# Optimization experiments

Measured on AMD Instinct MI355X. Metric: run time of the kernel, lower is better.

The kernel has to match this reference:

```python
import jax, jax.numpy as jnp
import numpy as np

B, P, ENC = 64, 49, 1280
T, V, E, H, A = 25, 10000, 512, 1024, 512


def setup_inputs() -> dict:
    key = jax.random.key(0)
    ks = jax.random.split(key, 20)
    s = 0.02
    return {
        "encoder_out": jax.random.normal(ks[0], (B, P, ENC), jnp.float32),
        "captions": jax.random.randint(ks[1], (B, T), 0, V, jnp.int32),
        "embed": jax.random.normal(ks[2], (V, E), jnp.float32) * s,
        "W_eatt": jax.random.normal(ks[3], (A, ENC), jnp.float32) * s,
        "b_eatt": jnp.zeros((A,), jnp.float32),
        "W_datt": jax.random.normal(ks[4], (A, H), jnp.float32) * s,
        "b_datt": jnp.zeros((A,), jnp.float32),
        "W_fatt": jax.random.normal(ks[5], (1, A), jnp.float32) * s,
        "b_fatt": jnp.zeros((1,), jnp.float32),
        "W_ih": jax.random.normal(ks[6], (4 * H, E + ENC), jnp.float32) * s,
        "b_ih": jnp.zeros((4 * H,), jnp.float32),
        "W_hh": jax.random.normal(ks[7], (4 * H, H), jnp.float32) * s,
        "b_hh": jnp.zeros((4 * H,), jnp.float32),
        "W_h0": jax.random.normal(ks[8], (H, ENC), jnp.float32) * s,
        "b_h0": jnp.zeros((H,), jnp.float32),
        "W_c0": jax.random.normal(ks[9], (H, ENC), jnp.float32) * s,
        "b_c0": jnp.zeros((H,), jnp.float32),
        "W_out": jax.random.normal(ks[10], (V, H), jnp.float32) * s,
        "b_out": jnp.zeros((V,), jnp.float32),
    }


def reference(encoder_out, captions, embed, W_eatt, b_eatt, W_datt, b_datt,
              W_fatt, b_fatt, W_ih, b_ih, W_hh, b_hh, W_h0, b_h0, W_c0, b_c0,
              W_out, b_out):
    emb = embed[captions]                       # [B,T,E]
    mean_enc = encoder_out.mean(axis=1)         # [B,ENC]
    h0 = mean_enc @ W_h0.T + b_h0               # [B,H]
    c0 = mean_enc @ W_c0.T + b_c0
    # encoder-side attention projection is step-invariant; hoist out of loop
    att1 = encoder_out @ W_eatt.T + b_eatt      # [B,P,A]
    nH = h0.shape[-1]

    def step(carry, x_t):
        h, c = carry
        att2 = h @ W_datt.T + b_datt                          # [B,A]
        e = (jax.nn.relu(att1 + att2[:, None, :]) @ W_fatt.T + b_fatt)[..., 0]  # [B,P]
        alpha = jax.nn.softmax(e, axis=1)
        ctx = jnp.einsum('bp,bpe->be', alpha, encoder_out)    # [B,ENC]
        gin = jnp.concatenate([x_t, ctx], axis=1)             # [B,E+ENC]
        gates = gin @ W_ih.T + b_ih + h @ W_hh.T + b_hh       # [B,4H]
        i, f, g, o = jnp.split(gates, 4, axis=1)
        c_new = jax.nn.sigmoid(f) * c + jax.nn.sigmoid(i) * jnp.tanh(g)
        h_new = jax.nn.sigmoid(o) * jnp.tanh(c_new)
        preds = h_new @ W_out.T + b_out                       # dropout in eval mode = identity
        return (h_new, c_new), preds

    xs = jnp.swapaxes(emb[:, :-1, :], 0, 1)     # [T-1,B,E]
    _, preds = jax.lax.scan(step, (h0, c0), xs)
    return jnp.swapaxes(preds, 0, 1)            # [B,T-1,V]
```

## Files before the change

### kernel.cpp

```cpp
#include <hip/hip_runtime.h>
#include <hip/hip_bf16.h>

typedef float  v4f __attribute__((ext_vector_type(4)));
typedef short  v8s __attribute__((ext_vector_type(8)));
typedef int    v4i __attribute__((ext_vector_type(4)));

#define DEV static __device__ __forceinline__

DEV float bf2f(unsigned short u) {
    union { unsigned int i; float f; } x; x.i = ((unsigned int)u) << 16; return x.f;
}
DEV unsigned short f2bf(float f) {
    union { float f; unsigned int i; } x; x.f = f;
    unsigned int r = x.i + 0x7fff + ((x.i >> 16) & 1);
    return (unsigned short)(r >> 16);
}
DEV float sigm(float x) { return 1.f / (1.f + __expf(-x)); }

__global__ __launch_bounds__(256) void uber_init(
    const float* __restrict__ Wih, const float* __restrict__ Whh,
    const float* __restrict__ bih, const float* __restrict__ bhh,
    const float* __restrict__ WoutF, const float* __restrict__ WeattF,
    const float* __restrict__ WdattF, const float* __restrict__ Wh0F,
    const float* __restrict__ Wc0F, const float* __restrict__ enc,
    const int* __restrict__ caps, const float* __restrict__ embed,
    unsigned short* __restrict__ Wz, unsigned short* __restrict__ Woutb,
    unsigned short* __restrict__ Weattb, unsigned short* __restrict__ Wdattb,
    unsigned short* __restrict__ Wh0b, unsigned short* __restrict__ Wc0b,
    unsigned short* __restrict__ encb, unsigned short* __restrict__ embb,
    unsigned short* __restrict__ meanb, float* __restrict__ bz)
{
    int i = blockIdx.x * 256 + threadIdx.x;
    if (i < 11534336) {
        int n = i / 2816, k = i - n * 2816;
        float v = (k < 1792) ? Wih[n * 1792 + k] : Whh[n * 1024 + (k - 1792)];
        Wz[i] = f2bf(v);
    } else if (i < 21774336) {
        int j = i - 11534336; Woutb[j] = f2bf(WoutF[j]);
    } else if (i < 22429696) {
        int j = i - 21774336; Weattb[j] = f2bf(WeattF[j]);
    } else if (i < 22953984) {
        int j = i - 22429696; Wdattb[j] = f2bf(WdattF[j]);
    } else if (i < 24264704) {
        int j = i - 22953984; Wh0b[j] = f2bf(Wh0F[j]);
    } else if (i < 25575424) {
        int j = i - 24264704; Wc0b[j] = f2bf(Wc0F[j]);
    } else if (i < 29589504) {
        int j = i - 25575424; encb[j] = f2bf(enc[j]);
    } else if (i < 30375936) {
        int j = i - 29589504;
        int b = j / 12288, r = j - b * 12288, t = r / 512, e = r - t * 512;
        embb[j] = f2bf(embed[caps[b * 25 + t] * 512 + e]);
    } else if (i < 30457856) {
        int j = i - 30375936;
        int b = j / 1280, c = j - b * 1280;
        float s = 0.f;
        for (int p = 0; p < 49; ++p) s += enc[(b * 49 + p) * 1280 + c];
        meanb[j] = f2bf(s * (1.f / 49.f));
    } else if (i < 30461952) {
        int j = i - 30457856; bz[j] = bih[j] + bhh[j];
    }
}

template <int OUT_BF16>
__global__ __launch_bounds__(256) void gemm64_bn16(
    const unsigned short* __restrict__ Ag, int lda,
    const unsigned short* __restrict__ Bg, int K,
    const float* __restrict__ bias, void* __restrict__ Cg, int ldc)
{
    __shared__ unsigned short lA[64 * 264];
    __shared__ unsigned short lB[16 * 264];
    const int tid = threadIdx.x, lane = tid & 63, w = tid >> 6;
    const int nb = blockIdx.x * 16;
    v4f acc = {0.f, 0.f, 0.f, 0.f};
    for (int kt = 0; kt < K; kt += 256) {
#pragma unroll
        for (int i = 0; i < 8; ++i) {
            int gid = i * 256 + tid, r = gid >> 5, c = (gid & 31) * 8;
            *(v4i*)&lA[r * 264 + c] = *(const v4i*)&Ag[r * lda + kt + c];
        }
#pragma unroll
        for (int i = 0; i < 2; ++i) {
            int gid = i * 256 + tid, r = gid >> 5, c = (gid & 31) * 8;
            *(v4i*)&lB[r * 264 + c] = *(const v4i*)&Bg[(nb + r) * K + kt + c];
        }
        __syncthreads();
#pragma unroll
        for (int ks = 0; ks < 8; ++ks) {
            v8s a = *(const v8s*)&lA[(w * 16 + (lane & 15)) * 264 + ks * 32 + (lane >> 4) * 8];
            v8s b = *(const v8s*)&lB[(lane & 15) * 264 + ks * 32 + (lane >> 4) * 8];
            acc = __builtin_amdgcn_mfma_f32_16x16x32_bf16(a, b, acc, 0, 0, 0);
        }
        __syncthreads();
    }
    const int n = nb + (lane & 15);
    const float bs = bias[n];
#pragma unroll
    for (int r = 0; r < 4; ++r) {
        int m = w * 16 + (lane >> 4) * 4 + r;
        float v = acc[r] + bs;
        if (OUT_BF16) ((unsigned short*)Cg)[m * ldc + n] = f2bf(v);
        else          ((float*)Cg)[m * ldc + n] = v;
    }
}

__global__ __launch_bounds__(256) void gemm_att1_k(
    const unsigned short* __restrict__ Aenc, const unsigned short* __restrict__ Bw,
    const float* __restrict__ bias, unsigned short* __restrict__ Cout)
{
    __shared__ unsigned short lA[64 * 136];
    __shared__ unsigned short lB[64 * 136];
    const int tid = threadIdx.x, lane = tid & 63, w = tid >> 6;
    const int mb = blockIdx.y * 64, nb = blockIdx.x * 64;
    v4f acc[4];
#pragma unroll
    for (int f = 0; f < 4; ++f) acc[f] = (v4f){0.f, 0.f, 0.f, 0.f};
    for (int kt = 0; kt < 1280; kt += 128) {
#pragma unroll
        for (int i = 0; i < 4; ++i) {
            int gid = i * 256 + tid, r = gid >> 4, c = (gid & 15) * 8;
            *(v4i*)&lA[r * 136 + c] = *(const v4i*)&Aenc[(mb + r) * 1280 + kt + c];
            *(v4i*)&lB[r * 136 + c] = *(const v4i*)&Bw[(nb + r) * 1280 + kt + c];
        }
        __syncthreads();
#pragma unroll
        for (int ks = 0; ks < 4; ++ks) {
            v8s a = *(const v8s*)&lA[(w * 16 + (lane & 15)) * 136 + ks * 32 + (lane >> 4) * 8];
#pragma unroll
            for (int f = 0; f < 4; ++f) {
                v8s b = *(const v8s*)&lB[(f * 16 + (lane & 15)) * 136 + ks * 32 + (lane >> 4) * 8];
                acc[f] = __builtin_amdgcn_mfma_f32_16x16x32_bf16(a, b, acc[f], 0, 0, 0);
            }
        }
        __syncthreads();
    }
#pragma unroll
    for (int f = 0; f < 4; ++f) {
        int n = nb + f * 16 + (lane & 15);
        float bs = bias[n];
#pragma unroll
        for (int r = 0; r < 4; ++r) {
            int m = mb + w * 16 + (lane >> 4) * 4 + r;
            Cout[m * 512 + n] = f2bf(acc[f][r] + bs);
        }
    }
}

__global__ __launch_bounds__(256) void attn_ctx_k(
    const float* __restrict__ att2, const unsigned short* __restrict__ att1b,
    const float* __restrict__ Wfatt, const float* __restrict__ bfatt,
    const unsigned short* __restrict__ encb, const unsigned short* __restrict__ embb,
    unsigned short* __restrict__ z, int tstep)
{
    __shared__ float a2[512];
    __shared__ float wf[512];
    __shared__ float es[64];
    __shared__ float alpha[64];
    const int tid = threadIdx.x, lane = tid & 63, w = tid >> 6;
    const int b = blockIdx.x;
    a2[tid]       = att2[b * 512 + tid];
    a2[tid + 256] = att2[b * 512 + tid + 256];
    wf[tid]       = Wfatt[tid];
    wf[tid + 256] = Wfatt[tid + 256];
    __syncthreads();
    for (int p = w; p < 49; p += 4) {
        float s = 0.f;
#pragma unroll
        for (int i = 0; i < 8; ++i) {
            int a = lane + i * 64;
            float v = bf2f(att1b[(b * 49 + p) * 512 + a]) + a2[a];
            s += fmaxf(v, 0.f) * wf[a];
        }
#pragma unroll
        for (int off = 32; off > 0; off >>= 1) s += __shfl_xor(s, off);
        if (lane == 0) es[p] = s + bfatt[0];
    }
    __syncthreads();
    if (w == 0) {
        float v = (lane < 49) ? es[lane] : -1e30f;
        float m = v;
#pragma unroll
        for (int off = 32; off > 0; off >>= 1) m = fmaxf(m, __shfl_xor(m, off));
        float e = (lane < 49) ? __expf(v - m) : 0.f;
        float s = e;
#pragma unroll
        for (int off = 32; off > 0; off >>= 1) s += __shfl_xor(s, off);
        if (lane < 49) alpha[lane] = e / s;
    }
    __syncthreads();
    for (int j = tid; j < 1280; j += 256) {
        float s = 0.f;
#pragma unroll
        for (int p = 0; p < 49; ++p)
            s += alpha[p] * bf2f(encb[(b * 49 + p) * 1280 + j]);
        z[b * 2816 + 512 + j] = f2bf(s);
    }
    for (int j = tid; j < 512; j += 256)
        z[b * 2816 + j] = embb[(b * 24 + tstep) * 512 + j];
}

__global__ __launch_bounds__(256) void gates_lstm_k(
    const unsigned short* __restrict__ z, const unsigned short* __restrict__ Wz,
    const float* __restrict__ bz, float* __restrict__ cst,
    unsigned short* __restrict__ zh, unsigned short* __restrict__ HallT)
{
    __shared__ unsigned short lA[64 * 264];
    __shared__ unsigned short lB[16 * 264];
    __shared__ float gbuf[64 * 20];
    const int tid = threadIdx.x, lane = tid & 63, w = tid >> 6;
    const int hb = blockIdx.x * 4;
    v4f acc = {0.f, 0.f, 0.f, 0.f};
    for (int kt = 0; kt < 2816; kt += 256) {
#pragma unroll
        for (int i = 0; i < 8; ++i) {
            int gid = i * 256 + tid, r = gid >> 5, c = (gid & 31) * 8;
            *(v4i*)&lA[r * 264 + c] = *(const v4i*)&z[r * 2816 + kt + c];
        }
#pragma unroll
        for (int i = 0; i < 2; ++i) {
            int gid = i * 256 + tid, r = gid >> 5, c = (gid & 31) * 8;
            int gate = r & 3, hco = r >> 2;
            int grow = gate * 1024 + hb + hco;
            *(v4i*)&lB[r * 264 + c] = *(const v4i*)&Wz[grow * 2816 + kt + c];
        }
        __syncthreads();
#pragma unroll
        for (int ks = 0; ks < 8; ++ks) {
            v8s a = *(const v8s*)&lA[(w * 16 + (lane & 15)) * 264 + ks * 32 + (lane >> 4) * 8];
            v8s b = *(const v8s*)&lB[(lane & 15) * 264 + ks * 32 + (lane >> 4) * 8];
            acc = __builtin_amdgcn_mfma_f32_16x16x32_bf16(a, b, acc, 0, 0, 0);
        }
        __syncthreads();
    }
#pragma unroll
    for (int r = 0; r < 4; ++r) {
        int m = w * 16 + (lane >> 4) * 4 + r;
        int n = lane & 15;
        gbuf[m * 20 + n] = acc[r];
    }
    __syncthreads();
    const int b = tid >> 2, hco = tid & 3, hidx = hb + hco;
    float gi = gbuf[b * 20 + hco * 4 + 0] + bz[hidx];
    float gf = gbuf[b * 20 + hco * 4 + 1] + bz[1024 + hidx];
    float gg = gbuf[b * 20 + hco * 4 + 2] + bz[2048 + hidx];
    float go = gbuf[b * 20 + hco * 4 + 3] + bz[3072 + hidx];
    float cn = sigm(gf) * cst[b * 1024 + hidx] + sigm(gi) * tanhf(gg);
    float hn = sigm(go) * tanhf(cn);
    cst[b * 1024 + hidx] = cn;
    unsigned short hb16 = f2bf(hn);
    zh[b * 2816 + hidx] = hb16;
    HallT[b * 1024 + hidx] = hb16;
}

__global__ __launch_bounds__(256) void preds_k(
    const unsigned short* __restrict__ Hall, const unsigned short* __restrict__ Wout,
    const float* __restrict__ bout, float* __restrict__ out)
{
    __shared__ unsigned short lA[128 * 72];
    __shared__ unsigned short lB[128 * 72];
    const int tid = threadIdx.x, lane = tid & 63, w = tid >> 6;
    const int mb = blockIdx.y * 128, nb = blockIdx.x * 128;
    v4f acc[2][8];
#pragma unroll
    for (int i = 0; i < 2; ++i)
#pragma unroll
        for (int f = 0; f < 8; ++f) acc[i][f] = (v4f){0.f, 0.f, 0.f, 0.f};
    for (int kt = 0; kt < 1024; kt += 64) {
#pragma unroll
        for (int i = 0; i < 4; ++i) {
            int gid = i * 256 + tid, r = gid >> 3, c = (gid & 7) * 8;
            *(v4i*)&lA[r * 72 + c] = *(const v4i*)&Hall[(mb + r) * 1024 + kt + c];
            int n = nb + r; if (n > 9999) n = 9999;
            *(v4i*)&lB[r * 72 + c] = *(const v4i*)&Wout[n * 1024 + kt + c];
        }
        __syncthreads();
#pragma unroll
        for (int ks = 0; ks < 2; ++ks) {
            int ko = ks * 32 + (lane >> 4) * 8;
            v8s a0 = *(const v8s*)&lA[(w * 32 + (lane & 15)) * 72 + ko];
            v8s a1 = *(const v8s*)&lA[(w * 32 + 16 + (lane & 15)) * 72 + ko];
#pragma unroll
            for (int f = 0; f < 8; ++f) {
                v8s b = *(const v8s*)&lB[(f * 16 + (lane & 15)) * 72 + ko];
                acc[0][f] = __builtin_amdgcn_mfma_f32_16x16x32_bf16(a0, b, acc[0][f], 0, 0, 0);
                acc[1][f] = __builtin_amdgcn_mfma_f32_16x16x32_bf16(a1, b, acc[1][f], 0, 0, 0);
            }
        }
        __syncthreads();
    }
#pragma unroll
    for (int f = 0; f < 8; ++f) {
        int n = nb + f * 16 + (lane & 15);
        if (n < 10000) {
            float bs = bout[n];
#pragma unroll
            for (int i = 0; i < 2; ++i)
#pragma unroll
                for (int r = 0; r < 4; ++r) {
                    int m = mb + w * 32 + i * 16 + (lane >> 4) * 4 + r;
                    int tt = m >> 6, bb = m & 63;
                    out[(bb * 24 + tt) * 10000 + n] = acc[i][f][r] + bs;
                }
        }
    }
}

extern "C" void kernel_launch(void* const* d_in, const int* in_sizes, int n_in,
                              void* d_out, int out_size, void* d_ws, size_t ws_size,
                              hipStream_t stream)
{
    const float* enc   = (const float*)d_in[0];
    const int*   caps  = (const int*)d_in[1];
    const float* embed = (const float*)d_in[2];
    const float* Weatt = (const float*)d_in[3];
    const float* beatt = (const float*)d_in[4];
    const float* Wdatt = (const float*)d_in[5];
    const float* bdatt = (const float*)d_in[6];
    const float* Wfatt = (const float*)d_in[7];
    const float* bfatt = (const float*)d_in[8];
    const float* Wih   = (const float*)d_in[9];
    const float* bih   = (const float*)d_in[10];
    const float* Whh   = (const float*)d_in[11];
    const float* bhh   = (const float*)d_in[12];
    const float* Wh0   = (const float*)d_in[13];
    const float* bh0   = (const float*)d_in[14];
    const float* Wc0   = (const float*)d_in[15];
    const float* bc0   = (const float*)d_in[16];
    const float* WoutF = (const float*)d_in[17];
    const float* bout  = (const float*)d_in[18];
    float* out = (float*)d_out;

    char* ws = (char*)d_ws;
    size_t off = 0;
    auto carve = [&](size_t bytes) -> void* {
        void* p = ws + off; off += (bytes + 255) & ~(size_t)255; return p;
    };
    unsigned short* Wzb    = (unsigned short*)carve(11534336ull * 2);
    unsigned short* Woutb  = (unsigned short*)carve(10240000ull * 2);
    unsigned short* Weattb = (unsigned short*)carve(655360ull * 2);
    unsigned short* Wdattb = (unsigned short*)carve(524288ull * 2);
    unsigned short* Wh0b   = (unsigned short*)carve(1310720ull * 2);
    unsigned short* Wc0b   = (unsigned short*)carve(1310720ull * 2);
    unsigned short* encb   = (unsigned short*)carve(4014080ull * 2);
    unsigned short* embb   = (unsigned short*)carve(786432ull * 2);
    unsigned short* meanb  = (unsigned short*)carve(81920ull * 2);
    unsigned short* att1b  = (unsigned short*)carve(1605632ull * 2);
    unsigned short* Hallb  = (unsigned short*)carve(1572864ull * 2);
    unsigned short* zb     = (unsigned short*)carve(180224ull * 2);
    float* bz   = (float*)carve(4096ull * 4);
    float* att2 = (float*)carve(32768ull * 4);
    float* cst  = (float*)carve(65536ull * 4);

    uber_init<<<118992, 256, 0, stream>>>(Wih, Whh, bih, bhh, WoutF, Weatt, Wdatt,
        Wh0, Wc0, enc, caps, embed, Wzb, Woutb, Weattb, Wdattb, Wh0b, Wc0b,
        encb, embb, meanb, bz);

    gemm64_bn16<1><<<64, 256, 0, stream>>>(meanb, 1280, Wh0b, 1280, bh0, zb + 1792, 2816);
    gemm64_bn16<0><<<64, 256, 0, stream>>>(meanb, 1280, Wc0b, 1280, bc0, cst, 1024);

    gemm_att1_k<<<dim3(8, 49), 256, 0, stream>>>(encb, Weattb, beatt, att1b);

    for (int t = 0; t < 24; ++t) {
        gemm64_bn16<0><<<32, 256, 0, stream>>>(zb + 1792, 2816, Wdattb, 1024, bdatt, att2, 512);
        attn_ctx_k<<<64, 256, 0, stream>>>(att2, att1b, Wfatt, bfatt, encb, embb, zb, t);
        gates_lstm_k<<<256, 256, 0, stream>>>(zb, Wzb, bz, cst, zb + 1792,
                                              Hallb + (size_t)t * 64 * 1024);
    }

    preds_k<<<dim3(79, 12), 256, 0, stream>>>(Hallb, Woutb, bout, out);
}
```

Measured before the change: 1.158 ms.

## Vectorize init conversion, register-prefetch GEMM tiles, vectorize attention loads

The init kernel now converts eight floats per thread with 128-bit loads and packed bf16 stores, cutting the grid size eightfold. All GEMM kernels (gemm64, att1, gates_lstm, preds) prefetch the next K tile into registers after the LDS barrier, so global loads overlap with MFMA work. The attention and context kernel reads bf16 data as 8-wide vectors and computes eight output columns per thread. The costs are higher register pressure and idle threads in the context phase.

```diff
diff --git a/kernel.cpp b/kernel.cpp
--- a/kernel.cpp
+++ b/kernel.cpp
@@ -16,6 +16,17 @@
     return (unsigned short)(r >> 16);
 }
 DEV float sigm(float x) { return 1.f / (1.f + __expf(-x)); }
+
+DEV v4i pack8(const float* f) {
+    v4i o;
+#pragma unroll
+    for (int q = 0; q < 4; ++q)
+        ((unsigned int*)&o)[q] = (unsigned int)f2bf(f[2 * q]) |
+                                 ((unsigned int)f2bf(f[2 * q + 1]) << 16);
+    return o;
+}
+DEV float lo16(unsigned int x) { union { unsigned int i; float f; } u; u.i = x << 16; return u.f; }
+DEV float hi16(unsigned int x) { union { unsigned int i; float f; } u; u.i = x & 0xffff0000u; return u.f; }
 
 __global__ __launch_bounds__(256) void uber_init(
     const float* __restrict__ Wih, const float* __restrict__ Whh,
@@ -30,35 +41,62 @@
     unsigned short* __restrict__ encb, unsigned short* __restrict__ embb,
     unsigned short* __restrict__ meanb, float* __restrict__ bz)
 {
-    int i = blockIdx.x * 256 + threadIdx.x;
+    const int i = (blockIdx.x * 256 + threadIdx.x) * 8;
+    float f[8];
     if (i < 11534336) {
         int n = i / 2816, k = i - n * 2816;
-        float v = (k < 1792) ? Wih[n * 1792 + k] : Whh[n * 1024 + (k - 1792)];
-        Wz[i] = f2bf(v);
+        const float* src = (k < 1792) ? &Wih[n * 1792 + k] : &Whh[n * 1024 + (k - 1792)];
+        *(v4f*)&f[0] = *(const v4f*)src; *(v4f*)&f[4] = *(const v4f*)(src + 4);
+        *(v4i*)&Wz[i] = pack8(f);
     } else if (i < 21774336) {
-        int j = i - 11534336; Woutb[j] = f2bf(WoutF[j]);
+        int j = i - 11534336;
+        *(v4f*)&f[0] = *(const v4f*)&WoutF[j]; *(v4f*)&f[4] = *(const v4f*)&WoutF[j + 4];
+        *(v4i*)&Woutb[j] = pack8(f);
     } else if (i < 22429696) {
-        int j = i - 21774336; Weattb[j] = f2bf(WeattF[j]);
+        int j = i - 21774336;
+        *(v4f*)&f[0] = *(const v4f*)&WeattF[j]; *(v4f*)&f[4] = *(const v4f*)&WeattF[j + 4];
+        *(v4i*)&Weattb[j] = pack8(f);
     } else if (i < 22953984) {
-        int j = i - 22429696; Wdattb[j] = f2bf(WdattF[j]);
+        int j = i - 22429696;
+        *(v4f*)&f[0] = *(const v4f*)&WdattF[j]; *(v4f*)&f[4] = *(const v4f*)&WdattF[j + 4];
+        *(v4i*)&Wdattb[j] = pack8(f);
     } else if (i < 24264704) {
-        int j = i - 22953984; Wh0b[j] = f2bf(Wh0F[j]);
+        int j = i - 22953984;
+        *(v4f*)&f[0] = *(const v4f*)&Wh0F[j]; *(v4f*)&f[4] = *(const v4f*)&Wh0F[j + 4];
+        *(v4i*)&Wh0b[j] = pack8(f);
     } else if (i < 25575424) {
-        int j = i - 24264704; Wc0b[j] = f2bf(Wc0F[j]);
+        int j = i - 24264704;
+        *(v4f*)&f[0] = *(const v4f*)&Wc0F[j]; *(v4f*)&f[4] = *(const v4f*)&Wc0F[j + 4];
+        *(v4i*)&Wc0b[j] = pack8(f);
     } else if (i < 29589504) {
-        int j = i - 25575424; encb[j] = f2bf(enc[j]);
+        int j = i - 25575424;
+        *(v4f*)&f[0] = *(const v4f*)&enc[j]; *(v4f*)&f[4] = *(const v4f*)&enc[j + 4];
+        *(v4i*)&encb[j] = pack8(f);
     } else if (i < 30375936) {
         int j = i - 29589504;
         int b = j / 12288, r = j - b * 12288, t = r / 512, e = r - t * 512;
-        embb[j] = f2bf(embed[caps[b * 25 + t] * 512 + e]);
+        const float* src = &embed[caps[b * 25 + t] * 512 + e];
+        *(v4f*)&f[0] = *(const v4f*)src; *(v4f*)&f[4] = *(const v4f*)(src + 4);
+        *(v4i*)&embb[j] = pack8(f);
     } else if (i < 30457856) {
         int j = i - 30375936;
         int b = j / 1280, c = j - b * 1280;
-        float s = 0.f;
-        for (int p = 0; p < 49; ++p) s += enc[(b * 49 + p) * 1280 + c];
-        meanb[j] = f2bf(s * (1.f / 49.f));
+#pragma unroll
+        for (int q = 0; q < 8; ++q) f[q] = 0.f;
+        for (int p = 0; p < 49; ++p) {
+            const float* src = &enc[(b * 49 + p) * 1280 + c];
+            v4f a = *(const v4f*)src, bq = *(const v4f*)(src + 4);
+#pragma unroll
+            for (int q = 0; q < 4; ++q) { f[q] += a[q]; f[q + 4] += bq[q]; }
+        }
+#pragma unroll
+        for (int q = 0; q < 8; ++q) f[q] *= (1.f / 49.f);
+        *(v4i*)&meanb[j] = pack8(f);
     } else if (i < 30461952) {
-        int j = i - 30457856; bz[j] = bih[j] + bhh[j];
+        int j = i - 30457856;
+#pragma unroll
+        for (int q = 0; q < 8; ++q) f[q] = bih[j + q] + bhh[j + q];
+        *(v4f*)&bz[j] = *(v4f*)&f[0]; *(v4f*)&bz[j + 4] = *(v4f*)&f[4];
     }
 }
 
@@ -72,19 +110,29 @@
     __shared__ unsigned short lB[16 * 264];
     const int tid = threadIdx.x, lane = tid & 63, w = tid >> 6;
     const int nb = blockIdx.x * 16;
+    const int rA = tid >> 5, cA = (tid & 31) * 8;
     v4f acc = {0.f, 0.f, 0.f, 0.f};
+    v4i ra[8], rb[2];
+#pragma unroll
+    for (int i = 0; i < 8; ++i)
+        ra[i] = *(const v4i*)&Ag[(rA + i * 8) * lda + cA];
+#pragma unroll
+    for (int i = 0; i < 2; ++i)
+        rb[i] = *(const v4i*)&Bg[(nb + rA + i * 8) * K + cA];
     for (int kt = 0; kt < K; kt += 256) {
 #pragma unroll
-        for (int i = 0; i < 8; ++i) {
-            int gid = i * 256 + tid, r = gid >> 5, c = (gid & 31) * 8;
-            *(v4i*)&lA[r * 264 + c] = *(const v4i*)&Ag[r * lda + kt + c];
-        }
-#pragma unroll
-        for (int i = 0; i < 2; ++i) {
-            int gid = i * 256 + tid, r = gid >> 5, c = (gid & 31) * 8;
-            *(v4i*)&lB[r * 264 + c] = *(const v4i*)&Bg[(nb + r) * K + kt + c];
-        }
-        __syncthreads();
+        for (int i = 0; i < 8; ++i) *(v4i*)&lA[(rA + i * 8) * 264 + cA] = ra[i];
+#pragma unroll
+        for (int i = 0; i < 2; ++i) *(v4i*)&lB[(rA + i * 8) * 264 + cA] = rb[i];
+        __syncthreads();
+        if (kt + 256 < K) {
+#pragma unroll
+            for (int i = 0; i < 8; ++i)
+                ra[i] = *(const v4i*)&Ag[(rA + i * 8) * lda + kt + 256 + cA];
+#pragma unroll
+            for (int i = 0; i < 2; ++i)
+                rb[i] = *(const v4i*)&Bg[(nb + rA + i * 8) * K + kt + 256 + cA];
+        }
 #pragma unroll
         for (int ks = 0; ks < 8; ++ks) {
             v8s a = *(const v8s*)&lA[(w * 16 + (lane & 15)) * 264 + ks * 32 + (lane >> 4) * 8];
@@ -112,17 +160,30 @@
     __shared__ unsigned short lB[64 * 136];
     const int tid = threadIdx.x, lane = tid & 63, w = tid >> 6;
     const int mb = blockIdx.y * 64, nb = blockIdx.x * 64;
+    const int rT = tid >> 4, cT = (tid & 15) * 8;
     v4f acc[4];
 #pragma unroll
     for (int f = 0; f < 4; ++f) acc[f] = (v4f){0.f, 0.f, 0.f, 0.f};
+    v4i ra[4], rb[4];
+#pragma unroll
+    for (int i = 0; i < 4; ++i) {
+        ra[i] = *(const v4i*)&Aenc[(mb + rT + i * 16) * 1280 + cT];
+        rb[i] = *(const v4i*)&Bw[(nb + rT + i * 16) * 1280 + cT];
+    }
     for (int kt = 0; kt < 1280; kt += 128) {
 #pragma unroll
         for (int i = 0; i < 4; ++i) {
-            int gid = i * 256 + tid, r = gid >> 4, c = (gid & 15) * 8;
-            *(v4i*)&lA[r * 136 + c] = *(const v4i*)&Aenc[(mb + r) * 1280 + kt + c];
-            *(v4i*)&lB[r * 136 + c] = *(const v4i*)&Bw[(nb + r) * 1280 + kt + c];
-        }
-        __syncthreads();
+            *(v4i*)&lA[(rT + i * 16) * 136 + cT] = ra[i];
+            *(v4i*)&lB[(rT + i * 16) * 136 + cT] = rb[i];
+        }
+        __syncthreads();
+        if (kt + 128 < 1280) {
+#pragma unroll
+            for (int i = 0; i < 4; ++i) {
+                ra[i] = *(const v4i*)&Aenc[(mb + rT + i * 16) * 1280 + kt + 128 + cT];
+                rb[i] = *(const v4i*)&Bw[(nb + rT + i * 16) * 1280 + kt + 128 + cT];
+            }
+        }
 #pragma unroll
         for (int ks = 0; ks < 4; ++ks) {
             v8s a = *(const v8s*)&lA[(w * 16 + (lane & 15)) * 136 + ks * 32 + (lane >> 4) * 8];
@@ -164,12 +225,20 @@
     wf[tid + 256] = Wfatt[tid + 256];
     __syncthreads();
     for (int p = w; p < 49; p += 4) {
+        v4i u = *(const v4i*)&att1b[(b * 49 + p) * 512 + lane * 8];
+        v4f c0 = *(const v4f*)&a2[lane * 8], c1 = *(const v4f*)&a2[lane * 8 + 4];
+        v4f w0 = *(const v4f*)&wf[lane * 8], w1 = *(const v4f*)&wf[lane * 8 + 4];
         float s = 0.f;
 #pragma unroll
-        for (int i = 0; i < 8; ++i) {
-            int a = lane + i * 64;
-            float v = bf2f(att1b[(b * 49 + p) * 512 + a]) + a2[a];
-            s += fmaxf(v, 0.f) * wf[a];
+        for (int q = 0; q < 4; ++q) {
+            unsigned int x = ((unsigned int*)&u)[q];
+            float vlo = lo16(x), vhi = hi16(x);
+            float clo = (q < 2) ? c0[q * 2] : c1[q * 2 - 4];
+            float chi = (q < 2) ? c0[q * 2 + 1] : c1[q * 2 - 3];
+            float wlo = (q < 2) ? w0[q * 2] : w1[q * 2 - 4];
+            float whi = (q < 2) ? w0[q * 2 + 1] : w1[q * 2 - 3];
+            s += fmaxf(vlo + clo, 0.f) * wlo;
+            s += fmaxf(vhi + chi, 0.f) * whi;
         }
 #pragma unroll
         for (int off = 32; off > 0; off >>= 1) s += __shfl_xor(s, off);
@@ -188,15 +257,25 @@
         if (lane < 49) alpha[lane] = e / s;
     }
     __syncthreads();
-    for (int j = tid; j < 1280; j += 256) {
-        float s = 0.f;
-#pragma unroll
-        for (int p = 0; p < 49; ++p)
-            s += alpha[p] * bf2f(encb[(b * 49 + p) * 1280 + j]);
-        z[b * 2816 + 512 + j] = f2bf(s);
-    }
-    for (int j = tid; j < 512; j += 256)
-        z[b * 2816 + j] = embb[(b * 24 + tstep) * 512 + j];
+    if (tid < 160) {
+        const int jb = tid * 8;
+        float acc[8];
+#pragma unroll
+        for (int q = 0; q < 8; ++q) acc[q] = 0.f;
+        for (int p = 0; p < 49; ++p) {
+            v4i u = *(const v4i*)&encb[(b * 49 + p) * 1280 + jb];
+            float al = alpha[p];
+#pragma unroll
+            for (int q = 0; q < 4; ++q) {
+                unsigned int x = ((unsigned int*)&u)[q];
+                acc[2 * q]     += al * lo16(x);
+                acc[2 * q + 1] += al * hi16(x);
+            }
+        }
+        *(v4i*)&z[b * 2816 + 512 + jb] = pack8(acc);
+    }
+    if (tid < 64)
+        *(v4i*)&z[b * 2816 + tid * 8] = *(const v4i*)&embb[(b * 24 + tstep) * 512 + tid * 8];
 }
 
 __global__ __launch_bounds__(256) void gates_lstm_k(
@@ -209,21 +288,30 @@
     __shared__ float gbuf[64 * 20];
     const int tid = threadIdx.x, lane = tid & 63, w = tid >> 6;
     const int hb = blockIdx.x * 4;
+    const int rT = tid >> 5, cT = (tid & 31) * 8;
+    const int gate = rT & 3, hco = rT >> 2;
+    const int growB = (gate * 1024 + hb + hco) * 2816;
+    const int growB2 = (((rT + 8) & 3) * 1024 + hb + ((rT + 8) >> 2)) * 2816;
     v4f acc = {0.f, 0.f, 0.f, 0.f};
+    v4i ra[8], rb[2];
+#pragma unroll
+    for (int i = 0; i < 8; ++i)
+        ra[i] = *(const v4i*)&z[(rT + i * 8) * 2816 + cT];
+    rb[0] = *(const v4i*)&Wz[growB + cT];
+    rb[1] = *(const v4i*)&Wz[growB2 + cT];
     for (int kt = 0; kt < 2816; kt += 256) {
 #pragma unroll
-        for (int i = 0; i < 8; ++i) {
-            int gid = i * 256 + tid, r = gid >> 5, c = (gid & 31) * 8;
-            *(v4i*)&lA[r * 264 + c] = *(const v4i*)&z[r * 2816 + kt + c];
-        }
-#pragma unroll
-        for (int i = 0; i < 2; ++i) {
-            int gid = i * 256 + tid, r = gid >> 5, c = (gid & 31) * 8;
-            int gate = r & 3, hco = r >> 2;
-            int grow = gate * 1024 + hb + hco;
-            *(v4i*)&lB[r * 264 + c] = *(const v4i*)&Wz[grow * 2816 + kt + c];
-        }
-        __syncthreads();
+        for (int i = 0; i < 8; ++i) *(v4i*)&lA[(rT + i * 8) * 264 + cT] = ra[i];
+        *(v4i*)&lB[rT * 264 + cT] = rb[0];
+        *(v4i*)&lB[(rT + 8) * 264 + cT] = rb[1];
+        __syncthreads();
+        if (kt + 256 < 2816) {
+#pragma unroll
+            for (int i = 0; i < 8; ++i)
+                ra[i] = *(const v4i*)&z[(rT + i * 8) * 2816 + kt + 256 + cT];
+            rb[0] = *(const v4i*)&Wz[growB + kt + 256 + cT];
+            rb[1] = *(const v4i*)&Wz[growB2 + kt + 256 + cT];
+        }
 #pragma unroll
         for (int ks = 0; ks < 8; ++ks) {
             v8s a = *(const v8s*)&lA[(w * 16 + (lane & 15)) * 264 + ks * 32 + (lane >> 4) * 8];
@@ -239,11 +327,11 @@
         gbuf[m * 20 + n] = acc[r];
     }
     __syncthreads();
-    const int b = tid >> 2, hco = tid & 3, hidx = hb + hco;
-    float gi = gbuf[b * 20 + hco * 4 + 0] + bz[hidx];
-    float gf = gbuf[b * 20 + hco * 4 + 1] + bz[1024 + hidx];
-    float gg = gbuf[b * 20 + hco * 4 + 2] + bz[2048 + hidx];
-    float go = gbuf[b * 20 + hco * 4 + 3] + bz[3072 + hidx];
+    const int b = tid >> 2, hc2 = tid & 3, hidx = hb + hc2;
+    float gi = gbuf[b * 20 + hc2 * 4 + 0] + bz[hidx];
+    float gf = gbuf[b * 20 + hc2 * 4 + 1] + bz[1024 + hidx];
+    float gg = gbuf[b * 20 + hc2 * 4 + 2] + bz[2048 + hidx];
+    float go = gbuf[b * 20 + hc2 * 4 + 3] + bz[3072 + hidx];
     float cn = sigm(gf) * cst[b * 1024 + hidx] + sigm(gi) * tanhf(gg);
     float hn = sigm(go) * tanhf(cn);
     cst[b * 1024 + hidx] = cn;
@@ -260,20 +348,35 @@
     __shared__ unsigned short lB[128 * 72];
     const int tid = threadIdx.x, lane = tid & 63, w = tid >> 6;
     const int mb = blockIdx.y * 128, nb = blockIdx.x * 128;
+    const int rT = tid >> 3, cT = (tid & 7) * 8;
+    int nB = nb + rT; if (nB > 9999) nB = 9999;
     v4f acc[2][8];
 #pragma unroll
     for (int i = 0; i < 2; ++i)
 #pragma unroll
         for (int f = 0; f < 8; ++f) acc[i][f] = (v4f){0.f, 0.f, 0.f, 0.f};
+    v4i ra[4], rb[4];
+#pragma unroll
+    for (int i = 0; i < 4; ++i) {
+        ra[i] = *(const v4i*)&Hall[(mb + rT + i * 32) * 1024 + cT];
+        int n2 = nb + rT + i * 32; if (n2 > 9999) n2 = 9999;
+        rb[i] = *(const v4i*)&Wout[n2 * 1024 + cT];
+    }
     for (int kt = 0; kt < 1024; kt += 64) {
 #pragma unroll
         for (int i = 0; i < 4; ++i) {
-            int gid = i * 256 + tid, r = gid >> 3, c = (gid & 7) * 8;
-            *(v4i*)&lA[r * 72 + c] = *(const v4i*)&Hall[(mb + r) * 1024 + kt + c];
-            int n = nb + r; if (n > 9999) n = 9999;
-            *(v4i*)&lB[r * 72 + c] = *(const v4i*)&Wout[n * 1024 + kt + c];
-        }
-        __syncthreads();
+            *(v4i*)&lA[(rT + i * 32) * 72 + cT] = ra[i];
+            *(v4i*)&lB[(rT + i * 32) * 72 + cT] = rb[i];
+        }
+        __syncthreads();
+        if (kt + 64 < 1024) {
+#pragma unroll
+            for (int i = 0; i < 4; ++i) {
+                ra[i] = *(const v4i*)&Hall[(mb + rT + i * 32) * 1024 + kt + 64 + cT];
+                int n2 = nb + rT + i * 32; if (n2 > 9999) n2 = 9999;
+                rb[i] = *(const v4i*)&Wout[n2 * 1024 + kt + 64 + cT];
+            }
+        }
 #pragma unroll
         for (int ks = 0; ks < 2; ++ks) {
             int ko = ks * 32 + (lane >> 4) * 8;
@@ -351,7 +454,7 @@
     float* att2 = (float*)carve(32768ull * 4);
     float* cst  = (float*)carve(65536ull * 4);
 
-    uber_init<<<118992, 256, 0, stream>>>(Wih, Whh, bih, bhh, WoutF, Weatt, Wdatt,
+    uber_init<<<14874, 256, 0, stream>>>(Wih, Whh, bih, bhh, WoutF, Weatt, Wdatt,
         Wh0, Wc0, enc, caps, embed, Wzb, Woutb, Weattb, Wdattb, Wh0b, Wc0b,
         encb, embb, meanb, bz);
 
```

New measurement: 1.137 ms. No clear change (-1.8%).
